# Kernel tuning notes

Measured on AMD Instinct MI355X. Metric: run time of the kernel, lower is better.

The kernel has to match this reference:

```python
import jax, jax.numpy as jnp
import numpy as np

N, DIM, HEADS, DH, WS = 32768, 1024, 8, 64, 256
INNER = HEADS * DH
MASK_VAL = -1e10  # ATTN_MASK_VALUE
EPS = 1e-5


def setup_inputs() -> dict:
    key = jax.random.key(0)
    k0, k1, k2 = jax.random.split(key, 3)
    x = jax.random.normal(k0, (N, DIM), jnp.float32)
    # rotary sin/cos with interleaved-pair layout matching rotate_every_two
    inv_freq = 1.0 / (10000.0 ** (jnp.arange(0, DH, 2, dtype=jnp.float32) / DH))
    freqs = jnp.arange(N, dtype=jnp.float32)[:, None] * inv_freq[None, :]  # [N, DH/2]
    sin = jnp.repeat(jnp.sin(freqs), 2, axis=-1)  # [N, DH]
    cos = jnp.repeat(jnp.cos(freqs), 2, axis=-1)  # [N, DH]
    gamma = jnp.ones((DIM,), jnp.float32)
    beta = jnp.zeros((DIM,), jnp.float32)
    w_qkv = jax.random.normal(k1, (DIM, 3 * INNER), jnp.float32) * 0.02
    w_out = jax.random.normal(k2, (INNER, DIM), jnp.float32) * 0.02
    b_out = jnp.zeros((DIM,), jnp.float32)
    return dict(x=x, sin=sin, cos=cos, gamma=gamma, beta=beta,
                w_qkv=w_qkv, w_out=w_out, b_out=b_out)


def _rotate_every_two(t):
    t1, t2 = t[..., 0::2], t[..., 1::2]
    return jnp.stack((-t2, t1), axis=-1).reshape(t.shape)


def _apply_rotary(t, sin, cos):
    # rot_dim == DH (full rotary), so no pass-through slice needed
    return t * cos + _rotate_every_two(t) * sin


def reference(x, sin, cos, gamma, beta, w_qkv, w_out, b_out):
    # LayerNorm (elementwise affine)
    mu = jnp.mean(x, axis=-1, keepdims=True)
    var = jnp.var(x, axis=-1, keepdims=True)
    x = (x - mu) * jax.lax.rsqrt(var + EPS) * gamma + beta
    # token shift: shift first half of channels by one token
    half = DIM // 2
    x_shift = jnp.pad(x[:, :half], ((1, 0), (0, 0)))[:-1]
    x = jnp.concatenate([x_shift, x[:, half:]], axis=-1)
    # qkv projection (no bias)
    qkv = x @ w_qkv  # [N, 3*INNER]
    q, k, v = jnp.split(qkv, 3, axis=-1)
    to_heads = lambda t: t.reshape(N, HEADS, DH).transpose(1, 0, 2)  # [H, N, DH]
    q, k, v = to_heads(q), to_heads(k), to_heads(v)
    # inline rotary on q, k AND v (as in source)
    q = _apply_rotary(q, sin, cos)
    k = _apply_rotary(k, sin, cos)
    v = _apply_rotary(v, sin, cos)
    # window split: [H, w, WS, DH]
    w = N // WS
    q, k, v = (t.reshape(HEADS, w, WS, DH) for t in (q, k, v))
    # look-back: each window attends to (previous window ++ current window)
    def lookback(t):
        t = jnp.pad(t, ((0, 0), (1, 0), (0, 0), (0, 0)))  # zero window at front
        return jnp.concatenate([t[:, :-1], t[:, 1:]], axis=2)  # [H, w, 2*WS, DH]
    k, v = lookback(k), lookback(v)
    sim = jnp.einsum('hwid,hwjd->hwij', q, k) * (DH ** -0.5)  # [H, w, WS, 2*WS]
    mask = jnp.tril(jnp.ones((WS, 2 * WS), dtype=bool), k=WS)  # j <= i + WS (causal)
    sim = jnp.where(mask, sim, MASK_VAL)
    attn = jax.nn.softmax(sim, axis=-1)
    out = jnp.einsum('hwij,hwjd->hwid', attn, v)  # [H, w, WS, DH]
    out = out.transpose(1, 2, 0, 3).reshape(N, INNER)  # '(w n) (h d)'
    return out @ w_out + b_out
```

## Files before the change

kernel.cpp:

```cpp
#include <hip/hip_runtime.h>

typedef __attribute__((ext_vector_type(4))) unsigned short us4;
typedef __attribute__((ext_vector_type(8))) unsigned short us8;
typedef __attribute__((ext_vector_type(8))) short s8;
typedef __attribute__((ext_vector_type(4))) float f32x4;
typedef __attribute__((ext_vector_type(16))) float f32x16;

#define NTOK 32768
#define DIM_ 1024
#define HEADS_ 8
#define DH_ 64
#define WS_ 256
#define NWIN_ 128
#define INNER_ 512

__device__ __forceinline__ float b2f(unsigned short u) {
  union { unsigned u; float f; } x; x.u = ((unsigned)u) << 16; return x.f;
}
__device__ __forceinline__ unsigned short f2b(float f) {
  union { float f; unsigned u; } x; x.f = f;
  unsigned r = x.u + 0x7FFFu + ((x.u >> 16) & 1u);
  return (unsigned short)(r >> 16);
}
__device__ __forceinline__ unsigned pk2(float a, float b) {
  return (unsigned)f2b(a) | ((unsigned)f2b(b) << 16);
}
__device__ __forceinline__ s8 mk_s8(unsigned w0, unsigned w1, unsigned w2, unsigned w3) {
  union { unsigned u[4]; s8 v; } x;
  x.u[0] = w0; x.u[1] = w1; x.u[2] = w2; x.u[3] = w3;
  return x.v;
}

__device__ __forceinline__ void gload_lds16(const unsigned short* g, void* l) {
  __builtin_amdgcn_global_load_lds((const __attribute__((address_space(1))) void*)g,
                                   (__attribute__((address_space(3))) void*)l, 16, 0, 0);
}

__global__ __launch_bounds__(256) void ln_shift(const float* __restrict__ x,
                                                const float* __restrict__ gamma,
                                                const float* __restrict__ beta,
                                                unsigned short* __restrict__ xs) {
  int row = blockIdx.x;
  int t = threadIdx.x;
  f32x4 v = ((const f32x4*)(x + (size_t)row * DIM_))[t];
  float sum = 0.f, ss = 0.f;
#pragma unroll
  for (int j = 0; j < 4; j++) { sum += v[j]; ss += v[j] * v[j]; }
#pragma unroll
  for (int off = 32; off >= 1; off >>= 1) {
    sum += __shfl_xor(sum, off);
    ss  += __shfl_xor(ss, off);
  }
  __shared__ float red[2][4];
  int wave = t >> 6, l = t & 63;
  if (l == 0) { red[0][wave] = sum; red[1][wave] = ss; }
  __syncthreads();
  sum = red[0][0] + red[0][1] + red[0][2] + red[0][3];
  ss  = red[1][0] + red[1][1] + red[1][2] + red[1][3];
  float mu = sum * (1.0f / DIM_);
  float var = ss * (1.0f / DIM_) - mu * mu;
  float rs = rsqrtf(var + 1e-5f);
  f32x4 g = ((const f32x4*)gamma)[t];
  f32x4 bb = ((const f32x4*)beta)[t];
  us4 o;
#pragma unroll
  for (int j = 0; j < 4; j++) o[j] = f2b((v[j] - mu) * rs * g[j] + bb[j]);
  int c0 = t * 4;
  if (c0 >= 512) {
    *(us4*)(xs + (size_t)row * DIM_ + c0) = o;
  } else {
    if (row + 1 < NTOK) *(us4*)(xs + (size_t)(row + 1) * DIM_ + c0) = o;
    if (row == 0) { us4 z = {0, 0, 0, 0}; *(us4*)(xs + c0) = z; }
  }
}

__global__ __launch_bounds__(256) void transpose_f32_bf16(const float* __restrict__ in,
                                                          unsigned short* __restrict__ out,
                                                          int R, int C) {
  __shared__ unsigned short tile[32][33];
  int bx = blockIdx.x * 32, by = blockIdx.y * 32;
  int tx = threadIdx.x, ty = threadIdx.y;
#pragma unroll
  for (int i = 0; i < 32; i += 8) tile[ty + i][tx] = f2b(in[(size_t)(by + ty + i) * C + bx + tx]);
  __syncthreads();
#pragma unroll
  for (int i = 0; i < 32; i += 8) out[(size_t)(bx + ty + i) * R + by + tx] = tile[tx][ty + i];
}

template <bool F32OUT>
__global__ __launch_bounds__(512, 2) void gemm_nt_p8(const unsigned short* __restrict__ A,
                                                     const unsigned short* __restrict__ Bt,
                                                     void* __restrict__ Cv,
                                                     const float* __restrict__ bias,
                                                     int M, int N, int K) {
  __shared__ __align__(16) char lds[131072];
  int t = threadIdx.x;
  int l = t & 63, lg = l >> 4, ll = l & 15;
  int wave = t >> 6;
  int wm = wave >> 2, wn = wave & 3;

  int nbx = gridDim.x;
  int nwg = nbx * gridDim.y;
  int flat = blockIdx.y * nbx + blockIdx.x;
  int swz = (flat & 7) * (nwg >> 3) + (flat >> 3);
  int m0 = (swz / nbx) * 256, n0 = (swz % nbx) * 256;

  const f32x4 fz = {0.f, 0.f, 0.f, 0.f};
  f32x4 acc[8][4];
#pragma unroll
  for (int m = 0; m < 8; m++)
#pragma unroll
    for (int n = 0; n < 4; n++) acc[m][n] = fz;

  int srow = t >> 3;
  int sunit = (t & 7) ^ (srow & 7);
  const unsigned short* gA = A + (size_t)(m0 + srow) * K + sunit * 8;
  const unsigned short* gB = Bt + (size_t)(n0 + srow) * K + sunit * 8;
  int t16 = t * 16;
  int nk = K >> 6;

#pragma unroll
  for (int j = 0; j < 4; j++) {
    gload_lds16(gA + (size_t)(j * 64) * K, lds + j * 8192 + t16);
    gload_lds16(gB + (size_t)(j * 64) * K, lds + 32768 + j * 8192 + t16);
  }

  for (int kt = 0; kt < nk - 1; ++kt) {
    const char* sa = lds + (kt & 1) * 65536;
    const char* sb = sa + 32768;
    char* dA = lds + ((kt + 1) & 1) * 65536;
    char* dB = dA + 32768;
    const unsigned short* nA = gA + (kt + 1) * 64;
    const unsigned short* nB = gB + (kt + 1) * 64;

    gload_lds16(nA, dA + t16);
    gload_lds16(nA + (size_t)64 * K, dA + 8192 + t16);
    asm volatile("s_waitcnt vmcnt(2)" ::: "memory");
    __builtin_amdgcn_sched_barrier(0);
    __builtin_amdgcn_s_barrier();
    __builtin_amdgcn_sched_barrier(0);

    s8 bf[4];
#pragma unroll
    for (int p = 0; p < 4; ++p) {
      const int qm = p & 1, kk = p >> 1;
      s8 af[4];
#pragma unroll
      for (int m = 0; m < 4; m++) {
        int r = wm * 128 + qm * 64 + m * 16 + ll;
        af[m] = *(const s8*)(sa + r * 128 + (((kk * 4 + lg) ^ (r & 7)) << 4));
      }
      if (qm == 0) {
#pragma unroll
        for (int n = 0; n < 4; n++) {
          int r = wn * 64 + n * 16 + ll;
          bf[n] = *(const s8*)(sb + r * 128 + (((kk * 4 + lg) ^ (r & 7)) << 4));
        }
      }
      if (p == 0) {
        gload_lds16(nA + (size_t)128 * K, dA + 16384 + t16);
        gload_lds16(nA + (size_t)192 * K, dA + 24576 + t16);
      } else if (p == 1) {
        gload_lds16(nB, dB + t16);
        gload_lds16(nB + (size_t)64 * K, dB + 8192 + t16);
      } else if (p == 2) {
        gload_lds16(nB + (size_t)128 * K, dB + 16384 + t16);
        gload_lds16(nB + (size_t)192 * K, dB + 24576 + t16);
      }
      __builtin_amdgcn_s_setprio(1);
#pragma unroll
      for (int m = 0; m < 4; m++)
#pragma unroll
        for (int n = 0; n < 4; n++)
          acc[qm * 4 + m][n] =
              __builtin_amdgcn_mfma_f32_16x16x32_bf16(af[m], bf[n], acc[qm * 4 + m][n], 0, 0, 0);
      __builtin_amdgcn_s_setprio(0);
    }
    __builtin_amdgcn_sched_barrier(0);
    __builtin_amdgcn_s_barrier();
  }

  {
    int kt = nk - 1;
    const char* sa = lds + (kt & 1) * 65536;
    const char* sb = sa + 32768;
    asm volatile("s_waitcnt vmcnt(0)" ::: "memory");
    __builtin_amdgcn_sched_barrier(0);
    __builtin_amdgcn_s_barrier();
    __builtin_amdgcn_sched_barrier(0);
    s8 bf[4];
#pragma unroll
    for (int p = 0; p < 4; ++p) {
      const int qm = p & 1, kk = p >> 1;
      s8 af[4];
#pragma unroll
      for (int m = 0; m < 4; m++) {
        int r = wm * 128 + qm * 64 + m * 16 + ll;
        af[m] = *(const s8*)(sa + r * 128 + (((kk * 4 + lg) ^ (r & 7)) << 4));
      }
      if (qm == 0) {
#pragma unroll
        for (int n = 0; n < 4; n++) {
          int r = wn * 64 + n * 16 + ll;
          bf[n] = *(const s8*)(sb + r * 128 + (((kk * 4 + lg) ^ (r & 7)) << 4));
        }
      }
#pragma unroll
      for (int m = 0; m < 4; m++)
#pragma unroll
        for (int n = 0; n < 4; n++)
          acc[qm * 4 + m][n] =
              __builtin_amdgcn_mfma_f32_16x16x32_bf16(af[m], bf[n], acc[qm * 4 + m][n], 0, 0, 0);
    }
  }

#pragma unroll
  for (int n = 0; n < 4; n++) {
    int col = n0 + wn * 64 + n * 16 + ll;
    float bs = bias ? bias[col] : 0.0f;
#pragma unroll
    for (int m = 0; m < 8; m++) {
#pragma unroll
      for (int r = 0; r < 4; r++) {
        int row = m0 + wm * 128 + m * 16 + lg * 4 + r;
        if (F32OUT) ((float*)Cv)[(size_t)row * N + col] = acc[m][n][r] + bs;
        else ((unsigned short*)Cv)[(size_t)row * N + col] = f2b(acc[m][n][r] + bs);
      }
    }
  }
}

__global__ __launch_bounds__(256) void rotary_qk(const unsigned short* __restrict__ qkv,
                                                 const float* __restrict__ sn,
                                                 const float* __restrict__ cs,
                                                 unsigned short* __restrict__ qh,
                                                 unsigned short* __restrict__ kh) {
  int gid = blockIdx.x * 256 + threadIdx.x;
  int n = gid >> 7;
  int col = (gid & 127) * 8;
  int d = col & 63;
  us8 v = *(const us8*)(qkv + (size_t)n * 1536 + col);
  float se[8], ce[8];
  *(f32x4*)se = *(const f32x4*)(sn + (size_t)n * 64 + d);
  *(f32x4*)(se + 4) = *(const f32x4*)(sn + (size_t)n * 64 + d + 4);
  *(f32x4*)ce = *(const f32x4*)(cs + (size_t)n * 64 + d);
  *(f32x4*)(ce + 4) = *(const f32x4*)(cs + (size_t)n * 64 + d + 4);
  us8 o;
#pragma unroll
  for (int p = 0; p < 4; p++) {
    float v0 = b2f(v[2 * p]), v1 = b2f(v[2 * p + 1]);
    o[2 * p]     = f2b(v0 * ce[2 * p] - v1 * se[2 * p]);
    o[2 * p + 1] = f2b(v1 * ce[2 * p + 1] + v0 * se[2 * p + 1]);
  }
  int third = col >> 9;
  int cw = col & 511;
  int h = cw >> 6;
  unsigned short* dst = third ? kh : qh;
  *(us8*)(dst + ((size_t)h * NTOK + n) * 64 + (cw & 63)) = o;
}

__global__ __launch_bounds__(256) void rotary_vT(const unsigned short* __restrict__ qkv,
                                                 const float* __restrict__ sn,
                                                 const float* __restrict__ cs,
                                                 unsigned short* __restrict__ vt) {
  __shared__ unsigned short tile[64][72];
  int nt = blockIdx.x, h = blockIdx.y;
  int t = threadIdx.x;
  int i = t >> 2;
  int cc = (t & 3) * 16;
  int n = nt * 64 + i;
  const unsigned short* src = qkv + (size_t)n * 1536 + 1024 + h * 64 + cc;
  us8 v0 = *(const us8*)src;
  us8 v1 = *(const us8*)(src + 8);
  float se[16], ce[16];
#pragma unroll
  for (int q = 0; q < 4; q++) {
    *(f32x4*)(se + 4 * q) = *(const f32x4*)(sn + (size_t)n * 64 + cc + 4 * q);
    *(f32x4*)(ce + 4 * q) = *(const f32x4*)(cs + (size_t)n * 64 + cc + 4 * q);
  }
#pragma unroll
  for (int p = 0; p < 4; p++) {
    float a0 = b2f(v0[2 * p]), a1 = b2f(v0[2 * p + 1]);
    tile[i][cc + 2 * p]     = f2b(a0 * ce[2 * p] - a1 * se[2 * p]);
    tile[i][cc + 2 * p + 1] = f2b(a1 * ce[2 * p + 1] + a0 * se[2 * p + 1]);
    float b0 = b2f(v1[2 * p]), b1 = b2f(v1[2 * p + 1]);
    tile[i][cc + 8 + 2 * p]     = f2b(b0 * ce[8 + 2 * p] - b1 * se[8 + 2 * p]);
    tile[i][cc + 8 + 2 * p + 1] = f2b(b1 * ce[8 + 2 * p + 1] + b0 * se[8 + 2 * p + 1]);
  }
  __syncthreads();
  int dd = t >> 2;
  int nc = (t & 3) * 16;
  us8 r0, r1;
#pragma unroll
  for (int j = 0; j < 8; j++) { r0[j] = tile[nc + j][dd]; r1[j] = tile[nc + 8 + j][dd]; }
  unsigned short* dst = vt + ((size_t)h * 64 + dd) * NTOK + (size_t)nt * 64 + nc;
  *(us8*)dst = r0;
  *(us8*)(dst + 8) = r1;
}

__global__ __launch_bounds__(256, 4) void attn_kernel(const unsigned short* __restrict__ qh,
                                                      const unsigned short* __restrict__ kh,
                                                      const unsigned short* __restrict__ vt,
                                                      unsigned short* __restrict__ ao) {
  __shared__ char kbuf[2][8192];
  __shared__ char vbuf[8192];
  int half = blockIdx.x, w = blockIdx.y, h = blockIdx.z;
  int t = threadIdx.x;
  int wave = t >> 6, l = t & 63;
  int l31 = l & 31, hi = l >> 5;
  const unsigned short* qb = qh + (size_t)h * NTOK * 64;
  const unsigned short* kb = kh + (size_t)h * NTOK * 64;
  const unsigned short* vb = vt + (size_t)h * 64 * NTOK;

  int qw = half * 128 + wave * 32 + l31;
  int qn = w * 256 + qw;
  s8 qf[4];
#pragma unroll
  for (int dht = 0; dht < 4; dht++)
    qf[dht] = *(const s8*)(qb + (size_t)qn * 64 + dht * 16 + hi * 8);

  f32x16 o0 = {}, o1 = {};
  float dsum = (w == 0) ? 128.f : 0.f;
  int n0 = w * 256 - 256;
  int c0 = (w == 0) ? 4 : 0;

  int srow = wave * 16 + (l >> 3);
  int sunit = l & 7;

  {
    const unsigned short* g = kb + (size_t)(n0 + c0 * 64 + srow) * 64 + ((sunit ^ (srow & 7)) * 8);
    gload_lds16(g, kbuf[c0 & 1] + wave * 2048);
    gload_lds16(g + 8 * 64, kbuf[c0 & 1] + wave * 2048 + 1024);
  }
  __syncthreads();

  for (int c = c0; c < 8; ++c) {
    int cb = n0 + c * 64;
    {
      int d = srow;
      const unsigned short* g = vb + (size_t)d * NTOK + cb + ((sunit ^ (d & 7)) * 8);
      gload_lds16(g, vbuf + wave * 2048);
      gload_lds16(g + (size_t)8 * NTOK, vbuf + wave * 2048 + 1024);
    }
    if (c < 7) {
      const unsigned short* g = kb + (size_t)(cb + 64 + srow) * 64 + ((sunit ^ (srow & 7)) * 8);
      gload_lds16(g, kbuf[(c + 1) & 1] + wave * 2048);
      gload_lds16(g + 8 * 64, kbuf[(c + 1) & 1] + wave * 2048 + 1024);
    }

    f32x16 s[2] = {{}, {}};
    const char* kl = kbuf[c & 1];
#pragma unroll
    for (int kt = 0; kt < 2; kt++) {
#pragma unroll
      for (int dht = 0; dht < 4; dht++) {
        int row = kt * 32 + l31;
        int unit = (dht * 2 + hi) ^ (row & 7);
        s8 kf = *(const s8*)(kl + row * 128 + unit * 16);
        s[kt] = __builtin_amdgcn_mfma_f32_32x32x16_bf16(kf, qf[dht], s[kt], 0, 0, 0);
      }
    }

    unsigned P0[2][4], P1[2][4];
#pragma unroll
    for (int kt = 0; kt < 2; kt++) {
#pragma unroll
      for (int r = 0; r < 16; r++) {
        int j = c * 64 + kt * 32 + (r & 3) + 8 * (r >> 2) + hi * 4;
        float e = (j <= qw + 256) ? __expf(s[kt][r] * 0.125f) : 0.f;
        s[kt][r] = e;
        dsum += e;
      }
#pragma unroll
      for (int j2 = 0; j2 < 4; j2++) {
        P0[kt][j2] = pk2(s[kt][j2 * 4 + 0], s[kt][j2 * 4 + 1]);
        P1[kt][j2] = pk2(s[kt][j2 * 4 + 2], s[kt][j2 * 4 + 3]);
      }
    }

    __syncthreads();

#pragma unroll
    for (int tt = 0; tt < 4; tt++) {
      int kt = tt >> 1, ss = tt & 1;
      unsigned a = P0[kt][2 * ss], b = P1[kt][2 * ss];
      unsigned cx = P0[kt][2 * ss + 1], dx = P1[kt][2 * ss + 1];
      asm volatile("v_permlane32_swap_b32 %0, %1" : "+v"(a), "+v"(cx));
      asm volatile("v_permlane32_swap_b32 %0, %1" : "+v"(b), "+v"(dx));
      s8 pf = mk_s8(a, b, cx, dx);
      {
        int row = l31;
        int unit = (tt * 2 + hi) ^ (row & 7);
        s8 vf = *(const s8*)(vbuf + row * 128 + unit * 16);
        o0 = __builtin_amdgcn_mfma_f32_32x32x16_bf16(vf, pf, o0, 0, 0, 0);
      }
      {
        int row = 32 + l31;
        int unit = (tt * 2 + hi) ^ (row & 7);
        s8 vf = *(const s8*)(vbuf + row * 128 + unit * 16);
        o1 = __builtin_amdgcn_mfma_f32_32x32x16_bf16(vf, pf, o1, 0, 0, 0);
      }
    }
    __syncthreads();
  }

  dsum += __shfl_xor(dsum, 32);
  float inv = 1.f / dsum;

  unsigned short* orow = ao + (size_t)qn * INNER_ + h * 64;
#pragma unroll
  for (int g = 0; g < 4; g++) {
    us4 st0, st1;
#pragma unroll
    for (int rr = 0; rr < 4; rr++) {
      st0[rr] = f2b(o0[g * 4 + rr] * inv);
      st1[rr] = f2b(o1[g * 4 + rr] * inv);
    }
    *(us4*)(orow + g * 8 + hi * 4) = st0;
    *(us4*)(orow + 32 + g * 8 + hi * 4) = st1;
  }
}

extern "C" void kernel_launch(void* const* d_in, const int* in_sizes, int n_in,
                              void* d_out, int out_size, void* d_ws, size_t ws_size,
                              hipStream_t stream) {
  const float* x     = (const float*)d_in[0];
  const float* sin_  = (const float*)d_in[1];
  const float* cos_  = (const float*)d_in[2];
  const float* gamma = (const float*)d_in[3];
  const float* beta  = (const float*)d_in[4];
  const float* w_qkv = (const float*)d_in[5];
  const float* w_out = (const float*)d_in[6];
  const float* b_out = (const float*)d_in[7];

  char* ws = (char*)d_ws;
  const size_t OFF_WQT = 0;
  const size_t OFF_WOT = 3145728;
  const size_t OFF_XS  = 4194304;
  const size_t OFF_QKV = 71303168;
  const size_t OFF_VT  = 171966464;
  const size_t NEEDED  = 205520896;
  if (ws_size < NEEDED) return;

  unsigned short* wqT = (unsigned short*)(ws + OFF_WQT);
  unsigned short* woT = (unsigned short*)(ws + OFF_WOT);
  unsigned short* xs  = (unsigned short*)(ws + OFF_XS);
  unsigned short* qkv = (unsigned short*)(ws + OFF_QKV);
  unsigned short* vt  = (unsigned short*)(ws + OFF_VT);
  unsigned short* qh  = xs;
  unsigned short* kh  = (unsigned short*)(ws + OFF_XS + 33554432);
  unsigned short* ao  = qkv;

  transpose_f32_bf16<<<dim3(1536 / 32, 1024 / 32), dim3(32, 8), 0, stream>>>(w_qkv, wqT, 1024, 1536);
  transpose_f32_bf16<<<dim3(1024 / 32, 512 / 32), dim3(32, 8), 0, stream>>>(w_out, woT, 512, 1024);
  ln_shift<<<NTOK, 256, 0, stream>>>(x, gamma, beta, xs);
  gemm_nt_p8<false><<<dim3(1536 / 256, NTOK / 256), 512, 0, stream>>>(xs, wqT, qkv, nullptr, NTOK, 1536, 1024);
  rotary_qk<<<(NTOK * 128) / 256, 256, 0, stream>>>(qkv, sin_, cos_, qh, kh);
  rotary_vT<<<dim3(NTOK / 64, HEADS_), 256, 0, stream>>>(qkv, sin_, cos_, vt);
  attn_kernel<<<dim3(2, NWIN_, HEADS_), 256, 0, stream>>>(qh, kh, vt, ao);
  gemm_nt_p8<true><<<dim3(1024 / 256, NTOK / 256), 512, 0, stream>>>(ao, woT, (void*)d_out, b_out, NTOK, 1024, 512);
}
```

Baseline: 342.9 us.

## Fuse rotary embedding and head/V-transpose scatter into QKV GEMM epilogue

```diff
diff --git a/kernel.cpp b/kernel.cpp
--- a/kernel.cpp
+++ b/kernel.cpp
@@ -87,12 +87,17 @@
   for (int i = 0; i < 32; i += 8) out[(size_t)(bx + ty + i) * R + by + tx] = tile[tx][ty + i];
 }
 
-template <bool F32OUT>
-__global__ __launch_bounds__(512, 2) void gemm_nt_p8(const unsigned short* __restrict__ A,
-                                                     const unsigned short* __restrict__ Bt,
-                                                     void* __restrict__ Cv,
-                                                     const float* __restrict__ bias,
-                                                     int M, int N, int K) {
+template <int MODE>
+__global__ __launch_bounds__(512, 2) void gemm_p10(const unsigned short* __restrict__ A,
+                                                   const unsigned short* __restrict__ Bt,
+                                                   void* __restrict__ Cv,
+                                                   const float* __restrict__ bias,
+                                                   const float* __restrict__ sinp,
+                                                   const float* __restrict__ cosp,
+                                                   unsigned short* __restrict__ qh,
+                                                   unsigned short* __restrict__ kh,
+                                                   unsigned short* __restrict__ vt,
+                                                   int M, int N, int K) {
   __shared__ __align__(16) char lds[131072];
   int t = threadIdx.x;
   int l = t & 63, lg = l >> 4, ll = l & 15;
@@ -214,88 +219,68 @@
     }
   }
 
-#pragma unroll
-  for (int n = 0; n < 4; n++) {
-    int col = n0 + wn * 64 + n * 16 + ll;
-    float bs = bias ? bias[col] : 0.0f;
+  if (MODE == 0) {
+    int b = ll & 3, q = ll >> 2;
+    int third = n0 >> 9;
+    bool bo1 = (b & 1) != 0, bo2 = (b & 2) != 0;
 #pragma unroll
     for (int m = 0; m < 8; m++) {
-#pragma unroll
-      for (int r = 0; r < 4; r++) {
-        int row = m0 + wm * 128 + m * 16 + lg * 4 + r;
-        if (F32OUT) ((float*)Cv)[(size_t)row * N + col] = acc[m][n][r] + bs;
-        else ((unsigned short*)Cv)[(size_t)row * N + col] = f2b(acc[m][n][r] + bs);
-      }
-    }
-  }
-}
-
-__global__ __launch_bounds__(256) void rotary_qk(const unsigned short* __restrict__ qkv,
-                                                 const float* __restrict__ sn,
-                                                 const float* __restrict__ cs,
-                                                 unsigned short* __restrict__ qh,
-                                                 unsigned short* __restrict__ kh) {
-  int gid = blockIdx.x * 256 + threadIdx.x;
-  int n = gid >> 7;
-  int col = (gid & 127) * 8;
-  int d = col & 63;
-  us8 v = *(const us8*)(qkv + (size_t)n * 1536 + col);
-  float se[8], ce[8];
-  *(f32x4*)se = *(const f32x4*)(sn + (size_t)n * 64 + d);
-  *(f32x4*)(se + 4) = *(const f32x4*)(sn + (size_t)n * 64 + d + 4);
-  *(f32x4*)ce = *(const f32x4*)(cs + (size_t)n * 64 + d);
-  *(f32x4*)(ce + 4) = *(const f32x4*)(cs + (size_t)n * 64 + d + 4);
-  us8 o;
-#pragma unroll
-  for (int p = 0; p < 4; p++) {
-    float v0 = b2f(v[2 * p]), v1 = b2f(v[2 * p + 1]);
-    o[2 * p]     = f2b(v0 * ce[2 * p] - v1 * se[2 * p]);
-    o[2 * p + 1] = f2b(v1 * ce[2 * p + 1] + v0 * se[2 * p + 1]);
-  }
-  int third = col >> 9;
-  int cw = col & 511;
-  int h = cw >> 6;
-  unsigned short* dst = third ? kh : qh;
-  *(us8*)(dst + ((size_t)h * NTOK + n) * 64 + (cw & 63)) = o;
-}
-
-__global__ __launch_bounds__(256) void rotary_vT(const unsigned short* __restrict__ qkv,
-                                                 const float* __restrict__ sn,
-                                                 const float* __restrict__ cs,
-                                                 unsigned short* __restrict__ vt) {
-  __shared__ unsigned short tile[64][72];
-  int nt = blockIdx.x, h = blockIdx.y;
-  int t = threadIdx.x;
-  int i = t >> 2;
-  int cc = (t & 3) * 16;
-  int n = nt * 64 + i;
-  const unsigned short* src = qkv + (size_t)n * 1536 + 1024 + h * 64 + cc;
-  us8 v0 = *(const us8*)src;
-  us8 v1 = *(const us8*)(src + 8);
-  float se[16], ce[16];
-#pragma unroll
-  for (int q = 0; q < 4; q++) {
-    *(f32x4*)(se + 4 * q) = *(const f32x4*)(sn + (size_t)n * 64 + cc + 4 * q);
-    *(f32x4*)(ce + 4 * q) = *(const f32x4*)(cs + (size_t)n * 64 + cc + 4 * q);
-  }
-#pragma unroll
-  for (int p = 0; p < 4; p++) {
-    float a0 = b2f(v0[2 * p]), a1 = b2f(v0[2 * p + 1]);
-    tile[i][cc + 2 * p]     = f2b(a0 * ce[2 * p] - a1 * se[2 * p]);
-    tile[i][cc + 2 * p + 1] = f2b(a1 * ce[2 * p + 1] + a0 * se[2 * p + 1]);
-    float b0 = b2f(v1[2 * p]), b1 = b2f(v1[2 * p + 1]);
-    tile[i][cc + 8 + 2 * p]     = f2b(b0 * ce[8 + 2 * p] - b1 * se[8 + 2 * p]);
-    tile[i][cc + 8 + 2 * p + 1] = f2b(b1 * ce[8 + 2 * p + 1] + b0 * se[8 + 2 * p + 1]);
-  }
-  __syncthreads();
-  int dd = t >> 2;
-  int nc = (t & 3) * 16;
-  us8 r0, r1;
-#pragma unroll
-  for (int j = 0; j < 8; j++) { r0[j] = tile[nc + j][dd]; r1[j] = tile[nc + 8 + j][dd]; }
-  unsigned short* dst = vt + ((size_t)h * 64 + dd) * NTOK + (size_t)nt * 64 + nc;
-  *(us8*)dst = r0;
-  *(us8*)(dst + 8) = r1;
+      int row = m0 + wm * 128 + m * 16 + lg * 4 + b;
+#pragma unroll
+      for (int n = 0; n < 4; n++) {
+        float v0 = acc[m][n][0], v1 = acc[m][n][1], v2 = acc[m][n][2], v3 = acc[m][n][3];
+        float x0 = __shfl_xor(v1, 1);
+        float x1 = __shfl_xor(v0, 1);
+        float x2 = __shfl_xor(v3, 1);
+        float x3 = __shfl_xor(v2, 1);
+        float u0 = bo1 ? x0 : v0;
+        float u1 = bo1 ? v1 : x1;
+        float u2 = bo1 ? x2 : v2;
+        float u3 = bo1 ? v3 : x3;
+        float y0 = __shfl_xor(u2, 2);
+        float y1 = __shfl_xor(u3, 2);
+        float y2 = __shfl_xor(u0, 2);
+        float y3 = __shfl_xor(u1, 2);
+        float w0 = bo2 ? y0 : u0;
+        float w1 = bo2 ? y1 : u1;
+        float w2 = bo2 ? u2 : y2;
+        float w3 = bo2 ? u3 : y3;
+        int cb = n0 + wn * 64 + n * 16 + q * 4;
+        int cit = cb & 511;
+        int head = cit >> 6, d0 = cit & 63;
+        f32x4 s4 = *(const f32x4*)(sinp + (size_t)row * 64 + d0);
+        f32x4 c4 = *(const f32x4*)(cosp + (size_t)row * 64 + d0);
+        us4 st;
+        st[0] = f2b(w0 * c4[0] - w1 * s4[0]);
+        st[1] = f2b(w1 * c4[1] + w0 * s4[1]);
+        st[2] = f2b(w2 * c4[2] - w3 * s4[2]);
+        st[3] = f2b(w3 * c4[3] + w2 * s4[3]);
+        if (third == 0) {
+          *(us4*)(qh + ((size_t)head * NTOK + row) * 64 + d0) = st;
+        } else if (third == 1) {
+          *(us4*)(kh + ((size_t)head * NTOK + row) * 64 + d0) = st;
+        } else {
+          unsigned short* vbase = vt + ((size_t)head * 64 + d0) * NTOK + row;
+#pragma unroll
+          for (int jj = 0; jj < 4; jj++) vbase[(size_t)jj * NTOK] = st[jj];
+        }
+      }
+    }
+  } else {
+#pragma unroll
+    for (int n = 0; n < 4; n++) {
+      int col = n0 + wn * 64 + n * 16 + ll;
+      float bs = bias ? bias[col] : 0.0f;
+#pragma unroll
+      for (int m = 0; m < 8; m++) {
+#pragma unroll
+        for (int r = 0; r < 4; r++) {
+          int row = m0 + wm * 128 + m * 16 + lg * 4 + r;
+          ((float*)Cv)[(size_t)row * N + col] = acc[m][n][r] + bs;
+        }
+      }
+    }
+  }
 }
 
 __global__ __launch_bounds__(256, 4) void attn_kernel(const unsigned short* __restrict__ qh,
@@ -437,26 +422,26 @@
   const size_t OFF_WQT = 0;
   const size_t OFF_WOT = 3145728;
   const size_t OFF_XS  = 4194304;
-  const size_t OFF_QKV = 71303168;
-  const size_t OFF_VT  = 171966464;
-  const size_t NEEDED  = 205520896;
+  const size_t OFF_QH  = 71303168;
+  const size_t OFF_KH  = 104857600;
+  const size_t OFF_VT  = 138412032;
+  const size_t NEEDED  = 171966464;
   if (ws_size < NEEDED) return;
 
   unsigned short* wqT = (unsigned short*)(ws + OFF_WQT);
   unsigned short* woT = (unsigned short*)(ws + OFF_WOT);
   unsigned short* xs  = (unsigned short*)(ws + OFF_XS);
-  unsigned short* qkv = (unsigned short*)(ws + OFF_QKV);
+  unsigned short* qh  = (unsigned short*)(ws + OFF_QH);
+  unsigned short* kh  = (unsigned short*)(ws + OFF_KH);
   unsigned short* vt  = (unsigned short*)(ws + OFF_VT);
-  unsigned short* qh  = xs;
-  unsigned short* kh  = (unsigned short*)(ws + OFF_XS + 33554432);
-  unsigned short* ao  = qkv;
+  unsigned short* ao  = xs;
 
   transpose_f32_bf16<<<dim3(1536 / 32, 1024 / 32), dim3(32, 8), 0, stream>>>(w_qkv, wqT, 1024, 1536);
   transpose_f32_bf16<<<dim3(1024 / 32, 512 / 32), dim3(32, 8), 0, stream>>>(w_out, woT, 512, 1024);
   ln_shift<<<NTOK, 256, 0, stream>>>(x, gamma, beta, xs);
-  gemm_nt_p8<false><<<dim3(1536 / 256, NTOK / 256), 512, 0, stream>>>(xs, wqT, qkv, nullptr, NTOK, 1536, 1024);
-  rotary_qk<<<(NTOK * 128) / 256, 256, 0, stream>>>(qkv, sin_, cos_, qh, kh);
-  rotary_vT<<<dim3(NTOK / 64, HEADS_), 256, 0, stream>>>(qkv, sin_, cos_, vt);
+  gemm_p10<0><<<dim3(1536 / 256, NTOK / 256), 512, 0, stream>>>(
+      xs, wqT, nullptr, nullptr, sin_, cos_, qh, kh, vt, NTOK, 1536, 1024);
   attn_kernel<<<dim3(2, NWIN_, HEADS_), 256, 0, stream>>>(qh, kh, vt, ao);
-  gemm_nt_p8<true><<<dim3(1024 / 256, NTOK / 256), 512, 0, stream>>>(ao, woT, (void*)d_out, b_out, NTOK, 1024, 512);
-}
+  gemm_p10<1><<<dim3(1024 / 256, NTOK / 256), 512, 0, stream>>>(
+      ao, woT, (void*)d_out, b_out, nullptr, nullptr, nullptr, nullptr, nullptr, NTOK, 1024, 512);
+}
```

Measured after the change: 333.2 us. 2.8% less time.
